# Optimization experiments

Measured on AMD Instinct MI355X. Metric: run time of the kernel, lower is better.

Reference implementation:

```python
import jax, jax.numpy as jnp
import numpy as np

SOFTCAP = 30.0  # final_logit_softcapping (Gemma2)


def setup_inputs() -> dict:
    key = jax.random.key(0)
    ks = jax.random.split(key, 6)
    B, S, D, V = 32, 8, 2048, 128000
    return {
        "embedding": jax.random.normal(ks[0], (V, D), jnp.float32) * 0.02,
        "hidden_states": jax.random.normal(ks[1], (B, S, D), jnp.float32),
        "temperatures": jax.random.uniform(ks[2], (B,), jnp.float32, 0.5, 1.0),
        "top_ps": jax.random.uniform(ks[3], (B,), jnp.float32, 0.5, 1.0),
        "output_positions": jax.random.randint(ks[4], (1,), 0, S),
        "top_ks": jax.random.randint(ks[5], (B,), 1, 64),
    }


def reference(embedding, hidden_states, temperatures, top_ps, output_positions, top_ks):
    # select decode position: [B, 1, D] -> [B, D]
    hs = jnp.take(hidden_states, output_positions, axis=1).squeeze(1)
    # logits over vocab: [B, V]
    logits = jnp.einsum("bd,vd->bv", hs, embedding)
    # final logit softcapping
    logits = jnp.tanh(logits / SOFTCAP) * SOFTCAP
    # temperature scaling (matches in-place div; returned logits are scaled)
    logits = logits / temperatures[:, None]
    probs = jax.nn.softmax(logits.astype(jnp.float32), axis=-1)
    # sort descending
    idx = jnp.argsort(-probs, axis=-1)                      # [B, V]
    probs_sort = jnp.take_along_axis(probs, idx, axis=-1)   # [B, V]
    cum = jnp.cumsum(probs_sort, axis=-1)
    V = probs.shape[-1]
    mask = ((cum - probs_sort) > top_ps[:, None]) | (
        jnp.arange(V)[None, :] >= top_ks[:, None]
    )
    probs_sort = jnp.where(mask, 0.0, probs_sort)
    probs_sort = probs_sort / probs_sort.sum(axis=-1, keepdims=True)
    # scatter back to vocab order
    inv = jnp.argsort(idx, axis=-1)
    probs_final = jnp.take_along_axis(probs_sort, inv, axis=-1)
    # multinomial sample (one draw per row)
    next_token_ids = jax.random.categorical(
        jax.random.key(42), jnp.log(probs_final), axis=-1
    )
    return next_token_ids, logits
```

## Files before the change

kernel.cpp:

```cpp
#include <hip/hip_runtime.h>
#include <float.h>
#include <math.h>

#define VOCAB 128000
#define DIM   2048
#define SEQL  8
#define NB    32
#define SCAP  4096

__device__ __forceinline__ unsigned f2sortable(float x){
  unsigned u = __float_as_uint(x);
  return (u & 0x80000000u) ? ~u : (u | 0x80000000u);
}
__device__ __forceinline__ unsigned rotl32(unsigned x, int d){
  return (x << d) | (x >> (32 - d));
}

__device__ float jax_gumbel(unsigned n){
  unsigned x0 = 0u, x1 = n;
  const unsigned k0 = 0u, k1 = 42u;
  const unsigned k2 = 0x1BD11BDAu ^ k0 ^ k1;
  x0 += k0; x1 += k1;
#define TFR(r) { x0 += x1; x1 = rotl32(x1, r); x1 ^= x0; }
  TFR(13) TFR(15) TFR(26) TFR(6)
  x0 += k1; x1 += k2 + 1u;
  TFR(17) TFR(29) TFR(16) TFR(24)
  x0 += k2; x1 += k0 + 2u;
  TFR(13) TFR(15) TFR(26) TFR(6)
  x0 += k0; x1 += k1 + 3u;
  TFR(17) TFR(29) TFR(16) TFR(24)
  x0 += k1; x1 += k2 + 4u;
  TFR(13) TFR(15) TFR(26) TFR(6)
  x0 += k2; x1 += k0 + 5u;
#undef TFR
  unsigned bits = x0 ^ x1;
  float f = __uint_as_float((bits >> 9) | 0x3f800000u) - 1.0f;
  float u = f + 1.17549435e-38f;
  return -logf(-logf(u));
}

__global__ __launch_bounds__(256, 4) void k_logits(
    const float* __restrict__ E, const float* __restrict__ HS,
    const float* __restrict__ temps, const int* __restrict__ posp,
    float* __restrict__ C)
{
  __shared__ float hs_s[2][NB * 64];
  __shared__ float tile[NB * 32];
  const int tid  = threadIdx.x;
  const int w    = tid >> 6;
  const int lane = tid & 63;
  const int g    = lane >> 4;
  const int qi   = lane & 15;
  const int pos  = posp[0];
  const int vbase = blockIdx.x * 32;
  const int vw    = vbase + w * 8;

  float acc[8][8];
#pragma unroll
  for (int j = 0; j < 8; ++j)
#pragma unroll
    for (int bl = 0; bl < 8; ++bl) acc[j][bl] = 0.f;

  const int sb0 = w * 8 + g;
  const int sb1 = w * 8 + 4 + g;
  const float* hsp0 = HS + ((size_t)(sb0 * SEQL + pos)) * DIM + qi * 4;
  const float* hsp1 = HS + ((size_t)(sb1 * SEQL + pos)) * DIM + qi * 4;
  const int lo0 = sb0 * 64 + qi * 4;
  const int lo1 = sb1 * 64 + qi * 4;

  {
    float4 a = *(const float4*)hsp0;
    float4 c = *(const float4*)hsp1;
    *(float4*)&hs_s[0][lo0] = a;
    *(float4*)&hs_s[0][lo1] = c;
  }

  const float* Eb = E + (size_t)vw * DIM + qi * 4;

  for (int s = 0; s < 32; ++s){
    __syncthreads();
    float4 e[8];
#pragma unroll
    for (int j = 0; j < 8; ++j)
      e[j] = *(const float4*)(Eb + (size_t)j * DIM + s * 64);
    float4 n0, n1;
    const bool more = (s + 1 < 32);
    if (more){
      n0 = *(const float4*)(hsp0 + (s + 1) * 64);
      n1 = *(const float4*)(hsp1 + (s + 1) * 64);
    }
    const float* hb = &hs_s[s & 1][0];
#pragma unroll
    for (int bl = 0; bl < 8; ++bl){
      float4 h = *(const float4*)(hb + (g * 8 + bl) * 64 + qi * 4);
#pragma unroll
      for (int j = 0; j < 8; ++j){
        acc[j][bl] = fmaf(e[j].x, h.x, acc[j][bl]);
        acc[j][bl] = fmaf(e[j].y, h.y, acc[j][bl]);
        acc[j][bl] = fmaf(e[j].z, h.z, acc[j][bl]);
        acc[j][bl] = fmaf(e[j].w, h.w, acc[j][bl]);
      }
    }
    if (more){
      float* wb = &hs_s[(s + 1) & 1][0];
      *(float4*)&wb[lo0] = n0;
      *(float4*)&wb[lo1] = n1;
    }
  }

#pragma unroll
  for (int j = 0; j < 8; ++j)
#pragma unroll
    for (int bl = 0; bl < 8; ++bl){
      float v = acc[j][bl];
      v += __shfl_xor(v, 1, 64);
      v += __shfl_xor(v, 2, 64);
      v += __shfl_xor(v, 4, 64);
      v += __shfl_xor(v, 8, 64);
      acc[j][bl] = v;
    }
  if (qi == 0){
#pragma unroll
    for (int j = 0; j < 8; ++j)
#pragma unroll
      for (int bl = 0; bl < 8; ++bl)
        tile[(g * 8 + bl) * 32 + w * 8 + j] = acc[j][bl];
  }
  __syncthreads();
  {
    const int b = tid >> 3, vq = tid & 7;
    const float tmp = temps[b];
    float4 tv = *(const float4*)&tile[b * 32 + vq * 4];
    float4 o;
    o.x = (tanhf(tv.x / 30.f) * 30.f) / tmp;
    o.y = (tanhf(tv.y / 30.f) * 30.f) / tmp;
    o.z = (tanhf(tv.z / 30.f) * 30.f) / tmp;
    o.w = (tanhf(tv.w / 30.f) * 30.f) / tmp;
    *(float4*)(C + (size_t)b * VOCAB + vbase + vq * 4) = o;
  }
}

__global__ __launch_bounds__(1024) void k_sample_fused(
    const float* __restrict__ C,
    const float* __restrict__ tps, const int* __restrict__ tks,
    float* __restrict__ out_tok)
{
  const int b = blockIdx.x, t = threadIdx.x;
  const float* row = C + (size_t)b * VOCAB;
  __shared__ float red[1024];
  __shared__ unsigned ps[1024];
  __shared__ unsigned hist[4096];
  __shared__ float    cval_s[SCAP];
  __shared__ int      cidx_s[SCAP];
  __shared__ int tbin_s;
  __shared__ unsigned cnt_s;

  if (t == 0) cnt_s = 0u;

  float m = -FLT_MAX;
  for (int f = t; f < VOCAB / 4; f += 1024){
    float4 x = ((const float4*)row)[f];
    m = fmaxf(m, fmaxf(fmaxf(x.x, x.y), fmaxf(x.z, x.w)));
  }
  red[t] = m; __syncthreads();
  for (int sft = 512; sft > 0; sft >>= 1){
    if (t < sft) red[t] = fmaxf(red[t], red[t + sft]);
    __syncthreads();
  }
  m = red[0];
  for (int i = t; i < 4096; i += 1024) hist[i] = 0u;
  __syncthreads();

  float zs = 0.f;
  for (int f = t; f < VOCAB / 4; f += 1024){
    float4 x4 = ((const float4*)row)[f];
    float xs[4] = {x4.x, x4.y, x4.z, x4.w};
#pragma unroll
    for (int c = 0; c < 4; ++c){
      zs += expf(xs[c] - m);
      atomicAdd(&hist[f2sortable(xs[c]) >> 20], 1u);
    }
  }
  red[t] = zs; __syncthreads();
  for (int sft = 512; sft > 0; sft >>= 1){
    if (t < sft) red[t] += red[t + sft];
    __syncthreads();
  }
  const float Z = red[0];

  unsigned s_t = 0u;
#pragma unroll
  for (int k = 0; k < 4; ++k) s_t += hist[t * 4 + k];
  ps[t] = s_t; __syncthreads();
  for (int off = 1; off < 1024; off <<= 1){
    unsigned v = ps[t] + ((t + off < 1024) ? ps[t + off] : 0u);
    __syncthreads();
    ps[t] = v;
    __syncthreads();
  }
  const unsigned Sstrict = ps[t] - s_t;
  if (Sstrict < 64u && ps[t] >= 64u){
    unsigned c = Sstrict;
    for (int bb = 3; bb >= 0; --bb){
      c += hist[t * 4 + bb];
      if (c >= 64u){ tbin_s = t * 4 + bb; break; }
    }
  }
  __syncthreads();
  const unsigned thr = ((unsigned)tbin_s) << 20;

  for (int f = t; f < VOCAB / 4; f += 1024){
    float4 x4 = ((const float4*)row)[f];
    float xs[4] = {x4.x, x4.y, x4.z, x4.w};
#pragma unroll
    for (int c = 0; c < 4; ++c){
      if (f2sortable(xs[c]) >= thr){
        unsigned slot = atomicAdd(&cnt_s, 1u);
        if (slot < (unsigned)SCAP){
          cval_s[slot] = xs[c];
          cidx_s[slot] = f * 4 + c;
        }
      }
    }
  }
  __syncthreads();
  int cn = (int)cnt_s; if (cn > SCAP) cn = SCAP;

  for (int j = t; j < cn; j += 1024)
    cval_s[j] = expf(cval_s[j] - m) / Z;
  __syncthreads();

  if (t < 64){
    float my_sp = 0.f; int my_si = 0;
    float lp = FLT_MAX; int li = -1;
    for (int r = 0; r < 64; ++r){
      float bp = -1.f; int bi = 0x7fffffff;
      for (int j = t; j < cn; j += 64){
        float p = cval_s[j]; int id = cidx_s[j];
        bool valid = (p < lp) || (p == lp && id > li);
        if (valid && (p > bp || (p == bp && id < bi))){ bp = p; bi = id; }
      }
#pragma unroll
      for (int off = 32; off >= 1; off >>= 1){
        float op = __shfl_xor(bp, off, 64);
        int   oi = __shfl_xor(bi, off, 64);
        if (op > bp || (op == bp && oi < bi)){ bp = op; bi = oi; }
      }
      if (t == r){ my_sp = bp; my_si = bi; }
      lp = bp; li = bi;
    }

    const float tp = tps[b];
    const int   tk = tks[b];
    float c = 0.f, sren = 0.f;
    bool keep_me = false;
    for (int j = 0; j < 64; ++j){
      float pj = __shfl(my_sp, j, 64);
      c = c + pj;
      float excl = c - pj;
      bool keep = (!(excl > tp)) && (j < tk);
      if (j == t) keep_me = keep;
      if (keep) sren = sren + pj;
    }

    float score = -FLT_MAX;
    int vid = my_si;
    if (keep_me){
      float pf = my_sp / sren;
      score = logf(pf) + jax_gumbel((unsigned)(b * VOCAB + vid));
    }
    float bs = score; int bv = vid;
#pragma unroll
    for (int off = 32; off >= 1; off >>= 1){
      float os = __shfl_xor(bs, off, 64);
      int   ov = __shfl_xor(bv, off, 64);
      if (os > bs || (os == bs && ov < bv)){ bs = os; bv = ov; }
    }
    if (t == 0) out_tok[b] = (float)bv;
  }
}

extern "C" void kernel_launch(void* const* d_in, const int* in_sizes, int n_in,
                              void* d_out, int out_size, void* d_ws, size_t ws_size,
                              hipStream_t stream)
{
  (void)in_sizes; (void)n_in; (void)out_size; (void)d_ws; (void)ws_size;
  const float* emb   = (const float*)d_in[0];
  const float* hs    = (const float*)d_in[1];
  const float* temps = (const float*)d_in[2];
  const float* tps   = (const float*)d_in[3];
  const int*   posp  = (const int*)d_in[4];
  const int*   tks   = (const int*)d_in[5];
  float* out = (float*)d_out;
  float* C   = out + NB;

  k_logits      <<<dim3(VOCAB / 32), dim3(256),  0, stream>>>(emb, hs, temps, posp, C);
  k_sample_fused<<<dim3(NB),         dim3(1024), 0, stream>>>(C, tps, tks, out);
}
```

Before: 429.3 us.

## Fuse row-max into logits kernel, async LDS loads, split embedding loads

The logits kernel now computes a per-row maximum via shuffles and a global atomicMax on sortable-encoded floats, so the sampling kernel no longer needs its first full pass over each 128k-entry row. The hidden-state double buffer is filled with global_load_lds direct-to-LDS loads instead of register staging. The embedding loads are split into two halves of four rows each to lower register pressure. This adds a memset and global atomics, and relies on the async LDS loads completing before the barrier.

```diff
diff --git a/kernel.cpp b/kernel.cpp
--- a/kernel.cpp
+++ b/kernel.cpp
@@ -12,8 +12,18 @@
   unsigned u = __float_as_uint(x);
   return (u & 0x80000000u) ? ~u : (u | 0x80000000u);
 }
+__device__ __forceinline__ float inv_sortable(unsigned u){
+  unsigned v = (u & 0x80000000u) ? (u ^ 0x80000000u) : ~u;
+  return __uint_as_float(v);
+}
 __device__ __forceinline__ unsigned rotl32(unsigned x, int d){
   return (x << d) | (x >> (32 - d));
+}
+__device__ __forceinline__ void gl_lds16(const float* g, float* l){
+  __builtin_amdgcn_global_load_lds(
+      (const __attribute__((address_space(1))) unsigned int*)g,
+      (__attribute__((address_space(3))) unsigned int*)l,
+      16, 0, 0);
 }
 
 __device__ float jax_gumbel(unsigned n){
@@ -42,7 +52,7 @@
 __global__ __launch_bounds__(256, 4) void k_logits(
     const float* __restrict__ E, const float* __restrict__ HS,
     const float* __restrict__ temps, const int* __restrict__ posp,
-    float* __restrict__ C)
+    float* __restrict__ C, unsigned* __restrict__ rowmax_u)
 {
   __shared__ float hs_s[2][NB * 64];
   __shared__ float tile[NB * 32];
@@ -61,50 +71,52 @@
 #pragma unroll
     for (int bl = 0; bl < 8; ++bl) acc[j][bl] = 0.f;
 
-  const int sb0 = w * 8 + g;
-  const int sb1 = w * 8 + 4 + g;
-  const float* hsp0 = HS + ((size_t)(sb0 * SEQL + pos)) * DIM + qi * 4;
-  const float* hsp1 = HS + ((size_t)(sb1 * SEQL + pos)) * DIM + qi * 4;
-  const int lo0 = sb0 * 64 + qi * 4;
-  const int lo1 = sb1 * 64 + qi * 4;
-
-  {
-    float4 a = *(const float4*)hsp0;
-    float4 c = *(const float4*)hsp1;
-    *(float4*)&hs_s[0][lo0] = a;
-    *(float4*)&hs_s[0][lo1] = c;
-  }
-
-  const float* Eb = E + (size_t)vw * DIM + qi * 4;
+  const int srow = w * 8 + (lane >> 4);
+  const float* src0 = HS + ((size_t)(srow * SEQL + pos)) * DIM + (qi << 2);
+  const float* src1 = HS + ((size_t)((srow + 4) * SEQL + pos)) * DIM + (qi << 2);
+
+  gl_lds16(src0, &hs_s[0][w * 512]);
+  gl_lds16(src1, &hs_s[0][w * 512 + 256]);
+
+  const float* Eb = E + (size_t)vw * DIM + (qi << 2);
 
   for (int s = 0; s < 32; ++s){
     __syncthreads();
-    float4 e[8];
-#pragma unroll
-    for (int j = 0; j < 8; ++j)
-      e[j] = *(const float4*)(Eb + (size_t)j * DIM + s * 64);
-    float4 n0, n1;
-    const bool more = (s + 1 < 32);
-    if (more){
-      n0 = *(const float4*)(hsp0 + (s + 1) * 64);
-      n1 = *(const float4*)(hsp1 + (s + 1) * 64);
-    }
-    const float* hb = &hs_s[s & 1][0];
+    if (s + 1 < 32){
+      float* dst = &hs_s[(s + 1) & 1][w * 512];
+      gl_lds16(src0 + (s + 1) * 64, dst);
+      gl_lds16(src1 + (s + 1) * 64, dst + 256);
+    }
+    const float* Ebs = Eb + s * 64;
+    const float* hb  = &hs_s[s & 1][0];
+    float4 e[4];
+#pragma unroll
+    for (int j = 0; j < 4; ++j)
+      e[j] = *(const float4*)(Ebs + (size_t)j * DIM);
 #pragma unroll
     for (int bl = 0; bl < 8; ++bl){
-      float4 h = *(const float4*)(hb + (g * 8 + bl) * 64 + qi * 4);
-#pragma unroll
-      for (int j = 0; j < 8; ++j){
+      float4 h = *(const float4*)(hb + (g * 8 + bl) * 64 + (qi << 2));
+#pragma unroll
+      for (int j = 0; j < 4; ++j){
         acc[j][bl] = fmaf(e[j].x, h.x, acc[j][bl]);
         acc[j][bl] = fmaf(e[j].y, h.y, acc[j][bl]);
         acc[j][bl] = fmaf(e[j].z, h.z, acc[j][bl]);
         acc[j][bl] = fmaf(e[j].w, h.w, acc[j][bl]);
       }
     }
-    if (more){
-      float* wb = &hs_s[(s + 1) & 1][0];
-      *(float4*)&wb[lo0] = n0;
-      *(float4*)&wb[lo1] = n1;
+#pragma unroll
+    for (int j = 0; j < 4; ++j)
+      e[j] = *(const float4*)(Ebs + (size_t)(j + 4) * DIM);
+#pragma unroll
+    for (int bl = 0; bl < 8; ++bl){
+      float4 h = *(const float4*)(hb + (g * 8 + bl) * 64 + (qi << 2));
+#pragma unroll
+      for (int j = 0; j < 4; ++j){
+        acc[j + 4][bl] = fmaf(e[j].x, h.x, acc[j + 4][bl]);
+        acc[j + 4][bl] = fmaf(e[j].y, h.y, acc[j + 4][bl]);
+        acc[j + 4][bl] = fmaf(e[j].z, h.z, acc[j + 4][bl]);
+        acc[j + 4][bl] = fmaf(e[j].w, h.w, acc[j + 4][bl]);
+      }
     }
   }
 
@@ -137,13 +149,18 @@
     o.z = (tanhf(tv.z / 30.f) * 30.f) / tmp;
     o.w = (tanhf(tv.w / 30.f) * 30.f) / tmp;
     *(float4*)(C + (size_t)b * VOCAB + vbase + vq * 4) = o;
+    float m4 = fmaxf(fmaxf(o.x, o.y), fmaxf(o.z, o.w));
+    m4 = fmaxf(m4, __shfl_xor(m4, 1, 64));
+    m4 = fmaxf(m4, __shfl_xor(m4, 2, 64));
+    m4 = fmaxf(m4, __shfl_xor(m4, 4, 64));
+    if (vq == 0) atomicMax(&rowmax_u[b], f2sortable(m4));
   }
 }
 
 __global__ __launch_bounds__(1024) void k_sample_fused(
     const float* __restrict__ C,
     const float* __restrict__ tps, const int* __restrict__ tks,
-    float* __restrict__ out_tok)
+    const unsigned* __restrict__ rowmax_u, float* __restrict__ out_tok)
 {
   const int b = blockIdx.x, t = threadIdx.x;
   const float* row = C + (size_t)b * VOCAB;
@@ -156,18 +173,7 @@
   __shared__ unsigned cnt_s;
 
   if (t == 0) cnt_s = 0u;
-
-  float m = -FLT_MAX;
-  for (int f = t; f < VOCAB / 4; f += 1024){
-    float4 x = ((const float4*)row)[f];
-    m = fmaxf(m, fmaxf(fmaxf(x.x, x.y), fmaxf(x.z, x.w)));
-  }
-  red[t] = m; __syncthreads();
-  for (int sft = 512; sft > 0; sft >>= 1){
-    if (t < sft) red[t] = fmaxf(red[t], red[t + sft]);
-    __syncthreads();
-  }
-  m = red[0];
+  const float m = inv_sortable(rowmax_u[b]);
   for (int i = t; i < 4096; i += 1024) hist[i] = 0u;
   __syncthreads();
 
@@ -284,7 +290,7 @@
                               void* d_out, int out_size, void* d_ws, size_t ws_size,
                               hipStream_t stream)
 {
-  (void)in_sizes; (void)n_in; (void)out_size; (void)d_ws; (void)ws_size;
+  (void)in_sizes; (void)n_in; (void)out_size; (void)ws_size;
   const float* emb   = (const float*)d_in[0];
   const float* hs    = (const float*)d_in[1];
   const float* temps = (const float*)d_in[2];
@@ -294,6 +300,9 @@
   float* out = (float*)d_out;
   float* C   = out + NB;
 
-  k_logits      <<<dim3(VOCAB / 32), dim3(256),  0, stream>>>(emb, hs, temps, posp, C);
-  k_sample_fused<<<dim3(NB),         dim3(1024), 0, stream>>>(C, tps, tks, out);
-}
+  unsigned* rowmax_u = (unsigned*)d_ws;
+  hipMemsetAsync(rowmax_u, 0, NB * sizeof(unsigned), stream);
+
+  k_logits      <<<dim3(VOCAB / 32), dim3(256),  0, stream>>>(emb, hs, temps, posp, C, rowmax_u);
+  k_sample_fused<<<dim3(NB),         dim3(1024), 0, stream>>>(C, tps, tks, rowmax_u, out);
+}
```

New measurement: 622.0 us. +44.9%, slower.
